# Performance work log

Hardware: AMD Instinct MI355X
Metric: run time of the kernel (lower is better)

Reference implementation:

```python
import jax, jax.numpy as jnp
import numpy as np

B, C, N, T = 16, 64, 512, 128


def setup_inputs() -> dict:
    key = jax.random.key(0)
    k1, k2, k3 = jax.random.split(key, 3)
    signals = jax.random.normal(k1, (B, C, N, T), dtype=jnp.float32)
    # learned parameters (original code leaves them uninitialized; use small randn)
    Wc = jax.random.normal(k2, (T, T), dtype=jnp.float32) * (1.0 / np.sqrt(T))
    alpha = jax.random.normal(k3, (N,), dtype=jnp.float32) * (1.0 / np.sqrt(N))
    return {"signals": signals, "Wc": Wc, "alpha": alpha}


def reference(signals, Wc, alpha):
    # k = q = sum_i signals[b,c,i,t] * alpha[i]  -> [B, C, T]
    k = jnp.einsum('bcit,i->bct', signals, alpha)
    # scores[b,c,c'] = k[b,c,:] @ Wc @ k[b,c',:]
    scores = jnp.einsum('bct,ts,bds->bcd', k, Wc, k)
    att = jax.nn.softmax(scores, axis=-1)  # [B, C, C]
    # mix channels: out[b,c,n,t] = sum_i att[b,c,i] * signals[b,i,n,t]
    return jnp.einsum('bci,bint->bcnt', att, signals)
```

## Files before the change

kernel.cpp:

```cpp
#include <hip/hip_runtime.h>
#include <hip/hip_bf16.h>
#include <math.h>

#define BB 16
#define CC 64
#define NN 512
#define TT 128
#define JJ (NN*TT)
#define JT 128

__global__ __launch_bounds__(256) void k_reduce_kernel(
    const float* __restrict__ sig, const float* __restrict__ alpha,
    float* __restrict__ kout)
{
    __shared__ float aS[NN];
    __shared__ float4 red[8][32];
    const int tid = threadIdx.x;
    for (int x = tid; x < NN; x += 256) aS[x] = alpha[x];
    __syncthreads();

    const int bc = blockIdx.x;
    const float* base = sig + (size_t)bc * (NN * TT);
    const int t4 = tid & 31;
    const int ig = tid >> 5;

    float4 acc = make_float4(0.f, 0.f, 0.f, 0.f);
    for (int i = ig; i < NN; i += 8) {
        float4 v = *(const float4*)(base + i * TT + t4 * 4);
        const float a = aS[i];
        acc.x = fmaf(v.x, a, acc.x);
        acc.y = fmaf(v.y, a, acc.y);
        acc.z = fmaf(v.z, a, acc.z);
        acc.w = fmaf(v.w, a, acc.w);
    }
    red[ig][t4] = acc;
    __syncthreads();
    if (tid < 32) {
        float4 s = red[0][tid];
        #pragma unroll
        for (int g = 1; g < 8; g++) {
            float4 r = red[g][tid];
            s.x += r.x; s.y += r.y; s.z += r.z; s.w += r.w;
        }
        *(float4*)(kout + (size_t)bc * TT + tid * 4) = s;
    }
}

__global__ __launch_bounds__(256) void kw_kernel(
    const float* __restrict__ kin, const float* __restrict__ Wc,
    float* __restrict__ kwT)
{
    __shared__ float kl[CC * TT];
    const int b = blockIdx.x;
    const int tid = threadIdx.x;
    const float* kb = kin + b * CC * TT;
    for (int x = tid; x < CC * TT; x += 256) kl[x] = kb[x];
    __syncthreads();

    float* kwb = kwT + b * TT * CC;
    for (int x = tid; x < CC * TT; x += 256) {
        const int c = x >> 7;
        const int s = x & 127;
        float acc = 0.f;
        for (int t = 0; t < TT; t++)
            acc = fmaf(kl[c * TT + t], Wc[t * TT + s], acc);
        kwb[s * CC + c] = acc;
    }
}

__global__ __launch_bounds__(256) void attn_kernel(
    const float* __restrict__ kin, const float* __restrict__ kwT,
    float* __restrict__ att)
{
    __shared__ float kw[TT * CC];
    __shared__ float sc[CC * 65];
    const int b = blockIdx.x;
    const int tid = threadIdx.x;
    const float* kwb = kwT + b * TT * CC;
    for (int x = tid; x < TT * CC; x += 256) kw[x] = kwb[x];
    __syncthreads();

    const float* kb = kin + b * CC * TT;
    for (int x = tid; x < CC * CC; x += 256) {
        const int c = x & 63;
        const int d = x >> 6;
        float acc = 0.f;
        for (int s = 0; s < TT; s++)
            acc = fmaf(kw[s * CC + c], kb[d * TT + s], acc);
        sc[c * 65 + d] = acc;
    }
    __syncthreads();

    if (tid < CC) {
        const int c = tid;
        float m = -1e30f;
        for (int d = 0; d < CC; d++) m = fmaxf(m, sc[c * 65 + d]);
        float sum = 0.f;
        for (int d = 0; d < CC; d++) {
            const float e = __expf(sc[c * 65 + d] - m);
            sc[c * 65 + d] = e;
            sum += e;
        }
        const float inv = 1.f / sum;
        float* ab = att + b * CC * CC + c * CC;
        for (int d = 0; d < CC; d++) ab[d] = sc[c * 65 + d] * inv;
    }
}

__global__ __launch_bounds__(256) void mix_kernel(
    const float* __restrict__ sig, const float* __restrict__ att,
    float* __restrict__ out)
{
    __shared__ float attL[CC][CC + 1];
    __shared__ float stile[CC][JT];
    const int b = blockIdx.y;
    const int jbase = blockIdx.x * JT;
    const int tid = threadIdx.x;

    const float* ab = att + b * CC * CC;
    for (int x = tid; x < CC * CC; x += 256)
        attL[x >> 6][x & 63] = ab[x];

    const float* sb = sig + (size_t)b * CC * JJ + jbase;
    for (int x = tid; x < CC * JT / 4; x += 256) {
        const int i = x >> 5;
        const int q = x & 31;
        *(float4*)(&stile[i][q * 4]) = *(const float4*)(sb + (size_t)i * JJ + q * 4);
    }
    __syncthreads();

    const int tc = tid >> 4;
    const int tj = tid & 15;

    float4 acc[4][2];
    #pragma unroll
    for (int q = 0; q < 4; q++) {
        acc[q][0] = make_float4(0.f, 0.f, 0.f, 0.f);
        acc[q][1] = make_float4(0.f, 0.f, 0.f, 0.f);
    }

    for (int i = 0; i < CC; i++) {
        float a[4];
        #pragma unroll
        for (int q = 0; q < 4; q++) a[q] = attL[4 * tc + q][i];
        #pragma unroll
        for (int u = 0; u < 2; u++) {
            const float4 s = *(const float4*)(&stile[i][(tj + 16 * u) * 4]);
            #pragma unroll
            for (int q = 0; q < 4; q++) {
                acc[q][u].x = fmaf(a[q], s.x, acc[q][u].x);
                acc[q][u].y = fmaf(a[q], s.y, acc[q][u].y);
                acc[q][u].z = fmaf(a[q], s.z, acc[q][u].z);
                acc[q][u].w = fmaf(a[q], s.w, acc[q][u].w);
            }
        }
    }

    float* ob = out + (size_t)b * CC * JJ + jbase;
    #pragma unroll
    for (int q = 0; q < 4; q++) {
        const int c = 4 * tc + q;
        #pragma unroll
        for (int u = 0; u < 2; u++)
            *(float4*)(ob + (size_t)c * JJ + (tj + 16 * u) * 4) = acc[q][u];
    }
}

extern "C" void kernel_launch(void* const* d_in, const int* in_sizes, int n_in,
                              void* d_out, int out_size, void* d_ws, size_t ws_size,
                              hipStream_t stream) {
    const float* sig   = (const float*)d_in[0];
    const float* Wc    = (const float*)d_in[1];
    const float* alpha = (const float*)d_in[2];
    float* out = (float*)d_out;

    float* k   = (float*)d_ws;
    float* kwT = k + BB * CC * TT;
    float* att = kwT + BB * TT * CC;

    k_reduce_kernel<<<BB * CC, 256, 0, stream>>>(sig, alpha, k);
    kw_kernel<<<BB, 256, 0, stream>>>(k, Wc, kwT);
    attn_kernel<<<BB, 256, 0, stream>>>(k, kwT, att);
    mix_kernel<<<dim3(JJ / JT, BB), 256, 0, stream>>>(sig, att, out);
}
```

Before: 604.5 us.

## Fuse kw and attention kernels into per-row blocks with wave-shuffle softmax

```diff
diff --git a/kernel.cpp b/kernel.cpp
--- a/kernel.cpp
+++ b/kernel.cpp
@@ -8,6 +8,7 @@
 #define TT 128
 #define JJ (NN*TT)
 #define JT 128
+#define KP 129
 
 __global__ __launch_bounds__(256) void k_reduce_kernel(
     const float* __restrict__ sig, const float* __restrict__ alpha,
@@ -46,64 +47,46 @@
     }
 }
 
-__global__ __launch_bounds__(256) void kw_kernel(
+__global__ __launch_bounds__(256) void attn_fused_kernel(
     const float* __restrict__ kin, const float* __restrict__ Wc,
-    float* __restrict__ kwT)
+    float* __restrict__ att)
 {
-    __shared__ float kl[CC * TT];
-    const int b = blockIdx.x;
+    __shared__ float kAll[CC * KP];
+    __shared__ float tmp[TT];
     const int tid = threadIdx.x;
+    const int b = blockIdx.x >> 6;
+    const int c = blockIdx.x & 63;
+
     const float* kb = kin + b * CC * TT;
-    for (int x = tid; x < CC * TT; x += 256) kl[x] = kb[x];
+    for (int x = tid; x < CC * TT; x += 256)
+        kAll[(x >> 7) * KP + (x & 127)] = kb[x];
     __syncthreads();
 
-    float* kwb = kwT + b * TT * CC;
-    for (int x = tid; x < CC * TT; x += 256) {
-        const int c = x >> 7;
-        const int s = x & 127;
+    if (tid < TT) {
         float acc = 0.f;
+        const float* kc = &kAll[c * KP];
         for (int t = 0; t < TT; t++)
-            acc = fmaf(kl[c * TT + t], Wc[t * TT + s], acc);
-        kwb[s * CC + c] = acc;
-    }
-}
-
-__global__ __launch_bounds__(256) void attn_kernel(
-    const float* __restrict__ kin, const float* __restrict__ kwT,
-    float* __restrict__ att)
-{
-    __shared__ float kw[TT * CC];
-    __shared__ float sc[CC * 65];
-    const int b = blockIdx.x;
-    const int tid = threadIdx.x;
-    const float* kwb = kwT + b * TT * CC;
-    for (int x = tid; x < TT * CC; x += 256) kw[x] = kwb[x];
-    __syncthreads();
-
-    const float* kb = kin + b * CC * TT;
-    for (int x = tid; x < CC * CC; x += 256) {
-        const int c = x & 63;
-        const int d = x >> 6;
-        float acc = 0.f;
-        for (int s = 0; s < TT; s++)
-            acc = fmaf(kw[s * CC + c], kb[d * TT + s], acc);
-        sc[c * 65 + d] = acc;
+            acc = fmaf(kc[t], Wc[t * TT + tid], acc);
+        tmp[tid] = acc;
     }
     __syncthreads();
 
     if (tid < CC) {
-        const int c = tid;
-        float m = -1e30f;
-        for (int d = 0; d < CC; d++) m = fmaxf(m, sc[c * 65 + d]);
-        float sum = 0.f;
-        for (int d = 0; d < CC; d++) {
-            const float e = __expf(sc[c * 65 + d] - m);
-            sc[c * 65 + d] = e;
-            sum += e;
-        }
-        const float inv = 1.f / sum;
-        float* ab = att + b * CC * CC + c * CC;
-        for (int d = 0; d < CC; d++) ab[d] = sc[c * 65 + d] * inv;
+        float acc = 0.f;
+        const float* kd = &kAll[tid * KP];
+        for (int s = 0; s < TT; s++)
+            acc = fmaf(tmp[s], kd[s], acc);
+
+        float m = acc;
+        #pragma unroll
+        for (int off = 32; off >= 1; off >>= 1)
+            m = fmaxf(m, __shfl_xor(m, off, 64));
+        const float e = __expf(acc - m);
+        float sum = e;
+        #pragma unroll
+        for (int off = 32; off >= 1; off >>= 1)
+            sum += __shfl_xor(sum, off, 64);
+        att[b * CC * CC + c * CC + tid] = e / sum;
     }
 }
 
@@ -111,7 +94,7 @@
     const float* __restrict__ sig, const float* __restrict__ att,
     float* __restrict__ out)
 {
-    __shared__ float attL[CC][CC + 1];
+    __shared__ float attT[CC * CC];
     __shared__ float stile[CC][JT];
     const int b = blockIdx.y;
     const int jbase = blockIdx.x * JT;
@@ -119,7 +102,7 @@
 
     const float* ab = att + b * CC * CC;
     for (int x = tid; x < CC * CC; x += 256)
-        attL[x >> 6][x & 63] = ab[x];
+        attT[(x & 63) * CC + (x >> 6)] = ab[x];
 
     const float* sb = sig + (size_t)b * CC * JJ + jbase;
     for (int x = tid; x < CC * JT / 4; x += 256) {
@@ -139,10 +122,10 @@
         acc[q][1] = make_float4(0.f, 0.f, 0.f, 0.f);
     }
 
+    #pragma unroll 4
     for (int i = 0; i < CC; i++) {
-        float a[4];
-        #pragma unroll
-        for (int q = 0; q < 4; q++) a[q] = attL[4 * tc + q][i];
+        const float4 a4 = *(const float4*)(&attT[i * CC + 4 * tc]);
+        const float a[4] = {a4.x, a4.y, a4.z, a4.w};
         #pragma unroll
         for (int u = 0; u < 2; u++) {
             const float4 s = *(const float4*)(&stile[i][(tj + 16 * u) * 4]);
@@ -175,11 +158,9 @@
     float* out = (float*)d_out;
 
     float* k   = (float*)d_ws;
-    float* kwT = k + BB * CC * TT;
-    float* att = kwT + BB * TT * CC;
+    float* att = k + BB * CC * TT;
 
     k_reduce_kernel<<<BB * CC, 256, 0, stream>>>(sig, alpha, k);
-    kw_kernel<<<BB, 256, 0, stream>>>(k, Wc, kwT);
-    attn_kernel<<<BB, 256, 0, stream>>>(k, kwT, att);
+    attn_fused_kernel<<<BB * CC, 256, 0, stream>>>(k, Wc, att);
     mix_kernel<<<dim3(JJ / JT, BB), 256, 0, stream>>>(sig, att, out);
 }
```

New measurement: 555.2 us. -8.2%, faster.
